# Optimization experiments

Hardware: AMD Instinct MI355X
Metric: run time of the kernel (lower is better)

## Reference

```python
import jax, jax.numpy as jnp
import numpy as np

B, S, D, H, KD, HID = 8, 1024, 512, 8, 64, 32


def setup_inputs() -> dict:
    key = jax.random.key(0)
    ks = jax.random.split(key, 13)
    s = 0.05
    return {
        "src": jax.random.normal(ks[0], (B, S, D), jnp.float32),
        "Wq": jax.random.normal(ks[1], (H, KD, D), jnp.float32) * s,
        "Wk": jax.random.normal(ks[2], (H, KD, D), jnp.float32) * s,
        "Wv": jax.random.normal(ks[3], (H, KD, D), jnp.float32) * s,
        "c_raw": jnp.ones((H,), jnp.float32),              # nn.Parameter(1.0) per head
        "L": jnp.full((H,), 2.0, jnp.float32),             # nn.Parameter(2.0) per head
        "w1": jax.random.normal(ks[4], (H, HID), jnp.float32) * s,   # Linear(1,HID) weight
        "b1": jax.random.normal(ks[5], (H, HID), jnp.float32) * s,
        "W2": jax.random.normal(ks[6], (H, HID, HID), jnp.float32) * s,  # [out,in]
        "b2": jax.random.normal(ks[7], (H, HID), jnp.float32) * s,
        "w3": jax.random.normal(ks[8], (H, HID), jnp.float32) * s,   # Linear(HID,1) weight
        "b3": jax.random.normal(ks[9], (H,), jnp.float32) * s,
        "Wo": jax.random.normal(ks[10], (D, D), jnp.float32) * s,
    }


def _gelu(x):
    return jax.nn.gelu(x, approximate=False)  # torch nn.GELU default (erf)


def reference(src, Wq, Wk, Wv, c_raw, L, w1, b1, W2, b2, w3, b3, Wo):
    Bc, Sc, Dc = src.shape
    Hh, Kd = Wq.shape[0], Wq.shape[1]
    # ---- FIRE bias: raw[i,j] = log1p(c*(i-j)) / log1p(c*max(L, i+1)) for j<i else 0
    ii = jnp.arange(Sc, dtype=jnp.float32)[:, None]   # [S,1]
    jj = jnp.arange(Sc, dtype=jnp.float32)[None, :]   # [1,S]
    d = ii - jj                                       # [S,S]
    c = jax.nn.softplus(c_raw)[:, None, None]         # [H,1,1]
    num = jnp.log1p(c * jnp.where(d > 0, d, 1.0)[None])          # safe for d<=0
    den = jnp.log1p(c * jnp.maximum(L[:, None, None], ii[None] + 1.0))
    raw = jnp.where(d[None] > 0, num / den, 0.0)      # [H,S,S]
    # ---- f_theta MLP applied elementwise (Linear(1,h)->GELU->Linear(h,h)->GELU->Linear(h,1))
    h1 = _gelu(raw[..., None] * w1[:, None, None, :] + b1[:, None, None, :])   # [H,S,S,HID]
    h2 = _gelu(jnp.einsum('hijk,hlk->hijl', h1, W2) + b2[:, None, None, :])    # [H,S,S,HID]
    bias = jnp.einsum('hijk,hk->hij', h2, w3) + b3[:, None, None]              # [H,S,S]
    # ---- causal mask (strict upper triangle -> -inf)
    causal = jnp.arange(Sc)[None, :] > jnp.arange(Sc)[:, None]
    bias = jnp.where(causal[None], -jnp.inf, bias)
    # ---- attention per head
    q = jnp.einsum('bsd,hkd->bhsk', src, Wq)
    k = jnp.einsum('bsd,hkd->bhsk', src, Wk)
    v = jnp.einsum('bsd,hkd->bhsk', src, Wv)
    logits = jnp.einsum('bhik,bhjk->bhij', q, k) / jnp.sqrt(jnp.float32(Kd)) + bias[None]
    attn = jax.nn.softmax(logits, axis=-1)
    o = jnp.einsum('bhij,bhjk->bhik', attn, v)        # [B,H,S,KD]
    o = jnp.transpose(o, (0, 2, 1, 3)).reshape(Bc, Sc, Hh * Kd)  # concat heads
    return o @ Wo.T
```

## Files before the change

kernel.cpp:

```cpp
#include <hip/hip_runtime.h>
#include <math.h>

#define S_LEN 1024
#define NHEAD 8
#define BATCH 8
#define KDIM  64
#define HID   32
#define NT    2048
#define LOG2E 1.4426950408889634f
#define TRI(q) ((q) * ((q) + 1) / 2)
#define PERM(m) (((m) & 0x20) | (((m) & 0x0C) << 1) | (((m) & 0x10) >> 2) | ((m) & 3))
#define SWZ(row) (((((row) >> 3) & 1) << 2) | ((row) & 3))

typedef __attribute__((ext_vector_type(8))) short bf16x8;
typedef __attribute__((ext_vector_type(4))) float f32x4;
typedef unsigned short ushort_t;

__device__ inline ushort_t f2bf(float f) {
  union { float f; unsigned u; } v; v.f = f;
  unsigned u = v.u;
  return (ushort_t)((u + 0x7FFFu + ((u >> 16) & 1u)) >> 16);
}
__device__ inline float bf2f(ushort_t u) {
  union { unsigned x; float f; } v; v.x = ((unsigned)u) << 16; return v.f;
}

__device__ inline void gl_lds16(const ushort_t* g, ushort_t* l) {
  __builtin_amdgcn_global_load_lds(
      (const __attribute__((address_space(1))) unsigned int*)g,
      (__attribute__((address_space(3))) unsigned int*)l, 16, 0, 0);
}

__global__ __launch_bounds__(256) void prep(
    const float* __restrict__ s, const float* __restrict__ wq,
    const float* __restrict__ wk, const float* __restrict__ wv,
    const float* __restrict__ wo,
    ushort_t* __restrict__ sb, ushort_t* __restrict__ wqb,
    ushort_t* __restrict__ wkb, ushort_t* __restrict__ wvb,
    ushort_t* __restrict__ wob,
    const float* __restrict__ c_raw, const float* __restrict__ Lp,
    const float* __restrict__ w1, const float* __restrict__ b1,
    const float* __restrict__ W2, const float* __restrict__ b2,
    const float* __restrict__ w3, const float* __restrict__ b3,
    float* __restrict__ num_g, float* __restrict__ rden_g,
    float* __restrict__ gtab_g) {
  __shared__ float h1s[8][33];
  const int bx = blockIdx.x;
  const int tid = threadIdx.x;
  if (bx < 5120) {
    const float* src; ushort_t* dst; int base; float scale = 1.0f;
    if (bx < 4096)      { src = s;  dst = sb;  base = bx; }
    else if (bx < 4352) { src = wq; dst = wqb; base = bx - 4096; scale = 0.125f * LOG2E; }
    else if (bx < 4608) { src = wk; dst = wkb; base = bx - 4352; }
    else if (bx < 4864) { src = wv; dst = wvb; base = bx - 4608; }
    else                { src = wo; dst = wob; base = bx - 4864; }
    const int i = (base * 256 + tid) * 4;
    float4 v = *(const float4*)&src[i];
    ushort4 o;
    o.x = f2bf(v.x * scale); o.y = f2bf(v.y * scale);
    o.z = f2bf(v.z * scale); o.w = f2bf(v.w * scale);
    *(ushort4*)&dst[i] = o;
  } else {
    const int idx = bx - 5120;
    const int h = idx / 257;
    const int xb = idx % 257;
    const float cr = c_raw[h];
    const float c = (cr > 20.f) ? cr : log1pf(expf(cr));
    const int gid = xb * 256 + tid;
    if (gid < S_LEN) {
      num_g[h * S_LEN + gid] = log1pf(c * (float)gid);
      rden_g[h * S_LEN + gid] = 1.0f / log1pf(c * fmaxf(Lp[h], (float)(gid + 1)));
    }
    const int pl = tid >> 5;
    const int j = tid & 31;
    const int pt = xb * 8 + pl;
    const float x = (float)pt * (1.0f / NT);
    float v = x * w1[h * HID + j] + b1[h * HID + j];
    h1s[pl][j] = 0.5f * v * (1.0f + erff(v * 0.70710678118f));
    __syncthreads();
    float sm = b2[h * HID + j];
    const float* w2r = W2 + ((size_t)(h * HID + j)) * HID;
    #pragma unroll
    for (int k = 0; k < HID; ++k) sm += w2r[k] * h1s[pl][k];
    float g = 0.5f * sm * (1.0f + erff(sm * 0.70710678118f));
    float y = w3[h * HID + j] * g;
    #pragma unroll
    for (int off = 1; off < 32; off <<= 1) y += __shfl_xor(y, off);
    if (j == 0 && pt <= NT) gtab_g[h * (NT + 1) + pt] = (y + b3[h]) * LOG2E;
  }
}

__device__ __forceinline__ void gemm_tile(
    ushort_t* sAB, const ushort_t* __restrict__ A, const ushort_t* __restrict__ Wp,
    void* __restrict__ outp, int mode, int m0, int n0, int tid) {
  ushort_t* sA = sAB;
  ushort_t* sB = sAB + 4096;
  const int lane = tid & 63, w = tid >> 6, quad = lane >> 4, l16 = lane & 15;
  f32x4 acc[4];
  #pragma unroll
  for (int nb = 0; nb < 4; ++nb) acc[nb] = (f32x4)0.0f;

  const int r8 = lane >> 3;
  const int gc = (lane & 7) ^ r8;
  const int sw = l16 & 7;

  for (int kt = 0; kt < 512; kt += 64) {
    __syncthreads();
    #pragma unroll
    for (int j = 0; j < 2; ++j) {
      const int row = w * 16 + j * 8 + r8;
      gl_lds16(&A[(size_t)(m0 + row) * 512 + kt + gc * 8], &sA[(w * 16 + j * 8) * 64]);
      gl_lds16(&Wp[(size_t)(n0 + row) * 512 + kt + gc * 8], &sB[(w * 16 + j * 8) * 64]);
    }
    __syncthreads();
    #pragma unroll
    for (int ks = 0; ks < 2; ++ks) {
      const int off = ((ks * 4 + quad) ^ sw) * 8;
      bf16x8 af = *(bf16x8*)&sA[(w * 16 + l16) * 64 + off];
      #pragma unroll
      for (int nb = 0; nb < 4; ++nb) {
        bf16x8 bfr = *(bf16x8*)&sB[(nb * 16 + l16) * 64 + off];
        acc[nb] = __builtin_amdgcn_mfma_f32_16x16x32_bf16(af, bfr, acc[nb], 0, 0, 0);
      }
    }
  }

  if (mode == 2) {
    __syncthreads();
    #pragma unroll
    for (int nb = 0; nb < 4; ++nb)
      #pragma unroll
      for (int r = 0; r < 4; ++r) {
        int nl = nb * 16 + l16;
        int ml = w * 16 + quad * 4 + r;
        sAB[nl * 64 + (((ml >> 3) ^ (nl & 7)) * 8) + (ml & 7)] = f2bf(acc[nb][r]);
      }
    __syncthreads();
    const int nl = tid >> 2, seg = tid & 3;
    const int ng = n0 + nl, hh = ng >> 6, kd = ng & 63;
    const int bb = m0 >> 10, sbase = m0 & 1023;
    ushort_t* vout = (ushort_t*)outp + (((size_t)(bb * NHEAD + hh)) * KDIM + kd) * S_LEN;
    #pragma unroll
    for (int c2 = 0; c2 < 2; ++c2) {
      int mc = seg * 2 + c2;
      bf16x8 vr = *(bf16x8*)&sAB[nl * 64 + ((mc ^ (nl & 7)) * 8)];
      *(bf16x8*)&vout[sbase + mc * 8] = vr;
    }
    return;
  }
  #pragma unroll
  for (int nb = 0; nb < 4; ++nb) {
    #pragma unroll
    for (int r = 0; r < 4; ++r) {
      int m = m0 + w * 16 + quad * 4 + r;
      int n = n0 + nb * 16 + l16;
      float v = acc[nb][r];
      if (mode == 1) {
        int bb = m >> 10, ss = m & 1023, hh = n >> 6, kd = n & 63;
        ((ushort_t*)outp)[(((size_t)(bb * NHEAD + hh)) * S_LEN + ss) * KDIM + kd] = f2bf(v);
      } else {
        ((float*)outp)[(size_t)m * 512 + n] = v;
      }
    }
  }
}

__global__ __launch_bounds__(256) void gemm_bias(
    const ushort_t* __restrict__ A,
    const ushort_t* __restrict__ W0, const ushort_t* __restrict__ W1,
    const ushort_t* __restrict__ W2w,
    void* __restrict__ out0, void* __restrict__ out1, void* __restrict__ out2,
    int scatter, int nGemm,
    const float* __restrict__ num_g, const float* __restrict__ rden_g,
    const float* __restrict__ gtab_g, ushort_t* __restrict__ biaspre) {
  __shared__ __align__(16) ushort_t sAB[8192];
  const int tid = threadIdx.x;
  if ((int)blockIdx.x < nGemm) {
    int z, tile;
    if (scatter) { z = blockIdx.x % 3; tile = blockIdx.x / 3; }
    else         { z = 0;              tile = blockIdx.x; }
    const int m0 = (tile & 127) * 64;
    const int n0 = (tile >> 7) * 64;
    const ushort_t* Wp = (z == 0) ? W0 : (z == 1) ? W1 : W2w;
    void* outp = (z == 0) ? out0 : (z == 1) ? out1 : out2;
    const int mode = scatter ? ((z == 2) ? 2 : 1) : 0;
    gemm_tile(sAB, A, Wp, outp, mode, m0, n0, tid);
  } else {
    const int idx = blockIdx.x - nGemm;
    const int h = idx / 68;
    const int pair = idx % 68;
    float* gtab_s = (float*)sAB;
    float* num_s = gtab_s + 2052;
    float* rden_s = num_s + 1024;
    for (int i = tid; i <= NT; i += 256) gtab_s[i] = gtab_g[h * (NT + 1) + i];
    for (int i = tid; i < S_LEN; i += 256) num_s[i] = num_g[h * S_LEN + i];
    const int sub = tid >> 7, tid2 = tid & 127;
    const int tileIdx = pair * 2 + sub;
    int qt = 0;
    while (TRI(qt + 1) <= tileIdx) ++qt;
    const int t = tileIdx - TRI(qt);
    if (tid2 < 64) rden_s[sub * 64 + tid2] = rden_g[h * S_LEN + qt * 64 + tid2];
    __syncthreads();
    const int w = tid2 >> 6, lane = tid2 & 63, quad = lane >> 4, l16 = lane & 15;
    ushort_t vals[32];
    #pragma unroll
    for (int qg = 0; qg < 2; ++qg) {
      const int iloc = w * 32 + qg * 16 + l16;
      const int i = qt * 64 + iloc;
      const float rden = rden_s[sub * 64 + iloc];
      #pragma unroll
      for (int nb = 0; nb < 4; ++nb)
        #pragma unroll
        for (int r = 0; r < 4; ++r) {
          const int m = nb * 16 + quad * 4 + r;
          const int j = t * 64 + PERM(m);
          ushort_t out;
          if (j > i) {
            out = 0xFF80;
          } else {
            const int d = i - j;
            float x = num_s[d] * rden;
            float tf = x * (float)NT;
            int it = (int)tf; it = it < (NT - 1) ? it : (NT - 1);
            float fr = tf - (float)it;
            float ga = gtab_s[it];
            out = f2bf(ga + (gtab_s[it + 1] - ga) * fr);
          }
          vals[qg * 16 + nb * 4 + r] = out;
        }
    }
    ushort_t* dst = &biaspre[((size_t)(h * 136 + tileIdx) * 128 + tid2) * 32];
    uint4 u[2];
    #pragma unroll
    for (int half = 0; half < 2; ++half) {
      #pragma unroll
      for (int v = 0; v < 8; ++v) ((ushort_t*)&u[0])[v] = vals[half * 16 + v];
      #pragma unroll
      for (int v = 0; v < 8; ++v) ((ushort_t*)&u[1])[v] = vals[half * 16 + 8 + v];
      *(uint4*)(dst + half * 16) = u[0];
      *(uint4*)(dst + half * 16 + 8) = u[1];
    }
  }
}

__global__ __launch_bounds__(128) void fire_attn_mfma(
    const ushort_t* __restrict__ Qg, const ushort_t* __restrict__ Kg,
    const ushort_t* __restrict__ Vtg, const ushort_t* __restrict__ biaspre,
    ushort_t* __restrict__ Ob) {
  __shared__ __align__(16) ushort_t Ks[64 * 64];
  __shared__ __align__(16) ushort_t Vt[64 * 64];
  const int tid = threadIdx.x;
  const int lane = tid & 63, w = tid >> 6, quad = lane >> 4, l16 = lane & 15;
  const int g = blockIdx.x >> 6;
  const int qt = (g < 8) ? (15 - g) : (g - 8);
  const int bh = blockIdx.x & 63, h = bh & 7, b = bh >> 3;

  bf16x8 q[2][2];
  {
    const size_t qb = (size_t)bh * S_LEN + qt * 64 + w * 32;
    #pragma unroll
    for (int qg = 0; qg < 2; ++qg)
      #pragma unroll
      for (int ks = 0; ks < 2; ++ks)
        q[qg][ks] = *(const bf16x8*)&Qg[(qb + qg * 16 + l16) * KDIM + ks * 32 + quad * 8];
  }

  const size_t kb = (size_t)bh * S_LEN * KDIM;
  const ushort_t* bptr = &biaspre[((size_t)(h * 136 + TRI(qt)) * 128 + tid) * 32];
  const int srow8 = lane >> 3;
  const int sc = lane & 7;

  f32x4 o[2][4];
  float ll[2] = {0.f, 0.f};
  #pragma unroll
  for (int qg = 0; qg < 2; ++qg)
    #pragma unroll
    for (int nb = 0; nb < 4; ++nb) o[qg][nb] = (f32x4)0.0f;

  for (int t = 0; t <= qt; ++t) {
    __syncthreads();
    #pragma unroll
    for (int j = 0; j < 4; ++j) {
      const int row = (w * 4 + j) * 8 + srow8;
      const int cc = sc ^ SWZ(row);
      gl_lds16(&Kg[kb + (size_t)(t * 64 + row) * 64 + cc * 8], &Ks[(w * 4 + j) * 512]);
      gl_lds16(&Vtg[kb + (size_t)row * 1024 + t * 64 + cc * 8], &Vt[(w * 4 + j) * 512]);
    }
    __syncthreads();

    uint4 bb0 = ((const uint4*)(bptr + (size_t)t * 4096))[0];
    uint4 bb1 = ((const uint4*)(bptr + (size_t)t * 4096))[1];
    uint4 bb2 = ((const uint4*)(bptr + (size_t)t * 4096))[2];
    uint4 bb3 = ((const uint4*)(bptr + (size_t)t * 4096))[3];

    f32x4 s[2][4];
    #pragma unroll
    for (int qg = 0; qg < 2; ++qg)
      #pragma unroll
      for (int nb = 0; nb < 4; ++nb) s[qg][nb] = (f32x4)0.0f;
    #pragma unroll
    for (int ks = 0; ks < 2; ++ks) {
      #pragma unroll
      for (int nb = 0; nb < 4; ++nb) {
        const int rk = PERM(nb * 16 + l16);
        bf16x8 ak = *(bf16x8*)&Ks[rk * 64 + (((ks * 4 + quad) ^ SWZ(rk)) * 8)];
        #pragma unroll
        for (int qg = 0; qg < 2; ++qg)
          s[qg][nb] = __builtin_amdgcn_mfma_f32_16x16x32_bf16(ak, q[qg][ks], s[qg][nb], 0, 0, 0);
      }
    }

    unsigned pk[2][4][2];
    #pragma unroll
    for (int qg = 0; qg < 2; ++qg) {
      #pragma unroll
      for (int nb = 0; nb < 4; ++nb) {
        const int v = qg * 16 + nb * 4;
        const uint4& bq = (v < 8) ? bb0 : (v < 16) ? bb1 : (v < 24) ? bb2 : bb3;
        const ushort_t* bu = (const ushort_t*)&bq;
        float p0 = __builtin_amdgcn_exp2f(s[qg][nb][0] + bf2f(bu[(v + 0) & 7]));
        float p1 = __builtin_amdgcn_exp2f(s[qg][nb][1] + bf2f(bu[(v + 1) & 7]));
        float p2 = __builtin_amdgcn_exp2f(s[qg][nb][2] + bf2f(bu[(v + 2) & 7]));
        float p3 = __builtin_amdgcn_exp2f(s[qg][nb][3] + bf2f(bu[(v + 3) & 7]));
        ll[qg] += (p0 + p1) + (p2 + p3);
        asm("v_cvt_pk_bf16_f32 %0, %1, %2" : "=v"(pk[qg][nb][0]) : "v"(p0), "v"(p1));
        asm("v_cvt_pk_bf16_f32 %0, %1, %2" : "=v"(pk[qg][nb][1]) : "v"(p2), "v"(p3));
      }
    }

    #pragma unroll
    for (int ks = 0; ks < 2; ++ks) {
      bf16x8 pf[2];
      #pragma unroll
      for (int qg = 0; qg < 2; ++qg) {
        union { bf16x8 v; unsigned u[4]; } pkx;
        pkx.u[0] = pk[qg][2 * ks][0];
        pkx.u[1] = pk[qg][2 * ks][1];
        pkx.u[2] = pk[qg][2 * ks + 1][0];
        pkx.u[3] = pk[qg][2 * ks + 1][1];
        pf[qg] = pkx.v;
      }
      #pragma unroll
      for (int nb = 0; nb < 4; ++nb) {
        const int rv = nb * 16 + l16;
        bf16x8 av = *(bf16x8*)&Vt[rv * 64 + (((ks * 4 + quad) ^ SWZ(rv)) * 8)];
        #pragma unroll
        for (int qg = 0; qg < 2; ++qg)
          o[qg][nb] = __builtin_amdgcn_mfma_f32_16x16x32_bf16(av, pf[qg], o[qg][nb], 0, 0, 0);
      }
    }
  }

  #pragma unroll
  for (int qg = 0; qg < 2; ++qg) {
    float rs = ll[qg];
    rs += __shfl_xor(rs, 16);
    rs += __shfl_xor(rs, 32);
    const float rl = 1.0f / rs;
    const size_t ob = ((size_t)(b * S_LEN + qt * 64 + w * 32 + qg * 16 + l16)) * 512 + h * KDIM;
    #pragma unroll
    for (int nb = 0; nb < 4; ++nb) {
      ushort4 ov;
      ov.x = f2bf(o[qg][nb][0] * rl);
      ov.y = f2bf(o[qg][nb][1] * rl);
      ov.z = f2bf(o[qg][nb][2] * rl);
      ov.w = f2bf(o[qg][nb][3] * rl);
      *(ushort4*)&Ob[ob + nb * 16 + quad * 4] = ov;
    }
  }
}

extern "C" void kernel_launch(void* const* d_in, const int* in_sizes, int n_in,
                              void* d_out, int out_size, void* d_ws, size_t ws_size,
                              hipStream_t stream) {
  const float* src   = (const float*)d_in[0];
  const float* Wq    = (const float*)d_in[1];
  const float* Wk    = (const float*)d_in[2];
  const float* Wv    = (const float*)d_in[3];
  const float* c_raw = (const float*)d_in[4];
  const float* Lp    = (const float*)d_in[5];
  const float* w1    = (const float*)d_in[6];
  const float* b1    = (const float*)d_in[7];
  const float* W2    = (const float*)d_in[8];
  const float* b2    = (const float*)d_in[9];
  const float* w3    = (const float*)d_in[10];
  const float* b3    = (const float*)d_in[11];
  const float* Wo    = (const float*)d_in[12];
  float* outp = (float*)d_out;

  const size_t SRC_E = 4194304;
  const size_t W_E   = 262144;
  const size_t QKV_E = 4194304;
  ushort_t* srcb = (ushort_t*)d_ws;
  ushort_t* Wqb  = srcb + SRC_E;
  ushort_t* Wkb  = Wqb + W_E;
  ushort_t* Wvb  = Wkb + W_E;
  ushort_t* Wob  = Wvb + W_E;
  ushort_t* Qb   = Wob + W_E;
  ushort_t* Kb   = Qb + QKV_E;
  ushort_t* Vtb  = Kb + QKV_E;
  ushort_t* Obb  = Vtb + QKV_E;
  ushort_t* biaspre = Obb + QKV_E;
  float* numb  = (float*)(biaspre + (size_t)NHEAD * 136 * 128 * 32);
  float* rdenb = numb + NHEAD * S_LEN;
  float* gtabb = rdenb + NHEAD * S_LEN;

  hipLaunchKernelGGL(prep, dim3(7176), dim3(256), 0, stream,
                     src, Wq, Wk, Wv, Wo, srcb, Wqb, Wkb, Wvb, Wob,
                     c_raw, Lp, w1, b1, W2, b2, w3, b3, numb, rdenb, gtabb);
  hipLaunchKernelGGL(gemm_bias, dim3(3616), dim3(256), 0, stream,
                     srcb, Wqb, Wkb, Wvb, (void*)Qb, (void*)Kb, (void*)Vtb,
                     1, 3072, numb, rdenb, gtabb, biaspre);
  hipLaunchKernelGGL(fire_attn_mfma, dim3(1024), dim3(128), 0, stream,
                     Qb, Kb, Vtb, biaspre, Obb);
  hipLaunchKernelGGL(gemm_bias, dim3(1024), dim3(256), 0, stream,
                     Obb, Wob, Wob, Wob, (void*)outp, (void*)outp, (void*)outp,
                     0, 1024, numb, rdenb, gtabb, biaspre);
}
```

Baseline: 167.0 us.

## Double-buffer LDS tiles in the projection GEMM and the attention K/V loop

Both the QKV/output GEMM tile loop and the attention K/V loop now use two LDS buffers. The next tile is issued with global-to-LDS loads while MFMA runs on the current tile, and each iteration needs one barrier instead of two. The aim is to hide global load latency behind compute. The cost is double the shared memory per block (32 KB in each kernel), which may lower the number of resident blocks per CU.

```diff
diff --git a/kernel.cpp b/kernel.cpp
--- a/kernel.cpp
+++ b/kernel.cpp
@@ -93,8 +93,6 @@
 __device__ __forceinline__ void gemm_tile(
     ushort_t* sAB, const ushort_t* __restrict__ A, const ushort_t* __restrict__ Wp,
     void* __restrict__ outp, int mode, int m0, int n0, int tid) {
-  ushort_t* sA = sAB;
-  ushort_t* sB = sAB + 4096;
   const int lane = tid & 63, w = tid >> 6, quad = lane >> 4, l16 = lane & 15;
   f32x4 acc[4];
   #pragma unroll
@@ -104,29 +102,38 @@
   const int gc = (lane & 7) ^ r8;
   const int sw = l16 & 7;
 
-  for (int kt = 0; kt < 512; kt += 64) {
-    __syncthreads();
+  auto stage = [&](int kt, int buf) {
+    ushort_t* sA = sAB + buf * 8192;
+    ushort_t* sB = sA + 4096;
     #pragma unroll
     for (int j = 0; j < 2; ++j) {
       const int row = w * 16 + j * 8 + r8;
       gl_lds16(&A[(size_t)(m0 + row) * 512 + kt + gc * 8], &sA[(w * 16 + j * 8) * 64]);
       gl_lds16(&Wp[(size_t)(n0 + row) * 512 + kt + gc * 8], &sB[(w * 16 + j * 8) * 64]);
     }
-    __syncthreads();
+  };
+
+  stage(0, 0);
+  __syncthreads();
+  for (int kt8 = 0; kt8 < 8; ++kt8) {
+    const int cur = kt8 & 1;
+    if (kt8 < 7) stage((kt8 + 1) * 64, cur ^ 1);
+    const ushort_t* sA = sAB + cur * 8192;
+    const ushort_t* sB = sA + 4096;
     #pragma unroll
     for (int ks = 0; ks < 2; ++ks) {
       const int off = ((ks * 4 + quad) ^ sw) * 8;
-      bf16x8 af = *(bf16x8*)&sA[(w * 16 + l16) * 64 + off];
+      bf16x8 af = *(const bf16x8*)&sA[(w * 16 + l16) * 64 + off];
       #pragma unroll
       for (int nb = 0; nb < 4; ++nb) {
-        bf16x8 bfr = *(bf16x8*)&sB[(nb * 16 + l16) * 64 + off];
+        bf16x8 bfr = *(const bf16x8*)&sB[(nb * 16 + l16) * 64 + off];
         acc[nb] = __builtin_amdgcn_mfma_f32_16x16x32_bf16(af, bfr, acc[nb], 0, 0, 0);
       }
     }
+    __syncthreads();
   }
 
   if (mode == 2) {
-    __syncthreads();
     #pragma unroll
     for (int nb = 0; nb < 4; ++nb)
       #pragma unroll
@@ -173,7 +180,7 @@
     int scatter, int nGemm,
     const float* __restrict__ num_g, const float* __restrict__ rden_g,
     const float* __restrict__ gtab_g, ushort_t* __restrict__ biaspre) {
-  __shared__ __align__(16) ushort_t sAB[8192];
+  __shared__ __align__(16) ushort_t sAB[16384];
   const int tid = threadIdx.x;
   if ((int)blockIdx.x < nGemm) {
     int z, tile;
@@ -247,8 +254,8 @@
     const ushort_t* __restrict__ Qg, const ushort_t* __restrict__ Kg,
     const ushort_t* __restrict__ Vtg, const ushort_t* __restrict__ biaspre,
     ushort_t* __restrict__ Ob) {
-  __shared__ __align__(16) ushort_t Ks[64 * 64];
-  __shared__ __align__(16) ushort_t Vt[64 * 64];
+  __shared__ __align__(16) ushort_t Ks[2 * 64 * 64];
+  __shared__ __align__(16) ushort_t Vt[2 * 64 * 64];
   const int tid = threadIdx.x;
   const int lane = tid & 63, w = tid >> 6, quad = lane >> 4, l16 = lane & 15;
   const int g = blockIdx.x >> 6;
@@ -270,6 +277,18 @@
   const int srow8 = lane >> 3;
   const int sc = lane & 7;
 
+  auto stageKV = [&](int t, int buf) {
+    #pragma unroll
+    for (int j = 0; j < 4; ++j) {
+      const int row = (w * 4 + j) * 8 + srow8;
+      const int cc = sc ^ SWZ(row);
+      gl_lds16(&Kg[kb + (size_t)(t * 64 + row) * 64 + cc * 8],
+               &Ks[buf * 4096 + (w * 4 + j) * 512]);
+      gl_lds16(&Vtg[kb + (size_t)row * 1024 + t * 64 + cc * 8],
+               &Vt[buf * 4096 + (w * 4 + j) * 512]);
+    }
+  };
+
   f32x4 o[2][4];
   float ll[2] = {0.f, 0.f};
   #pragma unroll
@@ -277,16 +296,13 @@
     #pragma unroll
     for (int nb = 0; nb < 4; ++nb) o[qg][nb] = (f32x4)0.0f;
 
+  stageKV(0, 0);
+  __syncthreads();
   for (int t = 0; t <= qt; ++t) {
-    __syncthreads();
-    #pragma unroll
-    for (int j = 0; j < 4; ++j) {
-      const int row = (w * 4 + j) * 8 + srow8;
-      const int cc = sc ^ SWZ(row);
-      gl_lds16(&Kg[kb + (size_t)(t * 64 + row) * 64 + cc * 8], &Ks[(w * 4 + j) * 512]);
-      gl_lds16(&Vtg[kb + (size_t)row * 1024 + t * 64 + cc * 8], &Vt[(w * 4 + j) * 512]);
-    }
-    __syncthreads();
+    const int cur = t & 1;
+    if (t < qt) stageKV(t + 1, cur ^ 1);
+    const ushort_t* Kc = Ks + cur * 4096;
+    const ushort_t* Vc = Vt + cur * 4096;
 
     uint4 bb0 = ((const uint4*)(bptr + (size_t)t * 4096))[0];
     uint4 bb1 = ((const uint4*)(bptr + (size_t)t * 4096))[1];
@@ -303,7 +319,7 @@
       #pragma unroll
       for (int nb = 0; nb < 4; ++nb) {
         const int rk = PERM(nb * 16 + l16);
-        bf16x8 ak = *(bf16x8*)&Ks[rk * 64 + (((ks * 4 + quad) ^ SWZ(rk)) * 8)];
+        bf16x8 ak = *(const bf16x8*)&Kc[rk * 64 + (((ks * 4 + quad) ^ SWZ(rk)) * 8)];
         #pragma unroll
         for (int qg = 0; qg < 2; ++qg)
           s[qg][nb] = __builtin_amdgcn_mfma_f32_16x16x32_bf16(ak, q[qg][ks], s[qg][nb], 0, 0, 0);
@@ -343,12 +359,13 @@
       #pragma unroll
       for (int nb = 0; nb < 4; ++nb) {
         const int rv = nb * 16 + l16;
-        bf16x8 av = *(bf16x8*)&Vt[rv * 64 + (((ks * 4 + quad) ^ SWZ(rv)) * 8)];
+        bf16x8 av = *(const bf16x8*)&Vc[rv * 64 + (((ks * 4 + quad) ^ SWZ(rv)) * 8)];
         #pragma unroll
         for (int qg = 0; qg < 2; ++qg)
           o[qg][nb] = __builtin_amdgcn_mfma_f32_16x16x32_bf16(av, pf[qg], o[qg][nb], 0, 0, 0);
       }
     }
+    __syncthreads();
   }
 
   #pragma unroll
```

Result: no change. 167.3 us (+0.2%).

## Split attention KV tiles across two wave pairs and merge partial sums in LDS

Applied to the files above, without the earlier changes.

The attention kernel now runs 256 threads per block. Two pairs of waves each handle half of the causal KV tiles for the same 64-row query tile, and the second pair's partial outputs and row sums are combined through shared memory at the end. The goal is to halve the serial KV loop length per block, which helps the long-tail query tiles and raises the number of waves available to hide latency. In exchange the block uses twice the LDS, adds a final reduction step, and leaves pair 1 idle on odd tile counts. This works without a running max because softmax here uses no max subtraction, so the partial sums add linearly.

```diff
diff --git a/kernel.cpp b/kernel.cpp
--- a/kernel.cpp
+++ b/kernel.cpp
@@ -23,6 +23,11 @@
 }
 __device__ inline float bf2f(ushort_t u) {
   union { unsigned x; float f; } v; v.x = ((unsigned)u) << 16; return v.f;
+}
+__device__ inline unsigned cvtpk_bf16(float lo, float hi) {
+  unsigned r;
+  asm("v_cvt_pk_bf16_f32 %0, %1, %2" : "=v"(r) : "v"(lo), "v"(hi));
+  return r;
 }
 
 __device__ inline void gl_lds16(const ushort_t* g, ushort_t* l) {
@@ -243,21 +248,23 @@
   }
 }
 
-__global__ __launch_bounds__(128) void fire_attn_mfma(
+__global__ __launch_bounds__(256) void fire_attn_mfma(
     const ushort_t* __restrict__ Qg, const ushort_t* __restrict__ Kg,
     const ushort_t* __restrict__ Vtg, const ushort_t* __restrict__ biaspre,
     ushort_t* __restrict__ Ob) {
-  __shared__ __align__(16) ushort_t Ks[64 * 64];
-  __shared__ __align__(16) ushort_t Vt[64 * 64];
+  __shared__ __align__(16) ushort_t sKV[16384];
   const int tid = threadIdx.x;
-  const int lane = tid & 63, w = tid >> 6, quad = lane >> 4, l16 = lane & 15;
+  const int lane = tid & 63, w = tid >> 6;
+  const int pair = w >> 1, wq = w & 1;
+  const int quad = lane >> 4, l16 = lane & 15;
   const int g = blockIdx.x >> 6;
   const int qt = (g < 8) ? (15 - g) : (g - 8);
   const int bh = blockIdx.x & 63, h = bh & 7, b = bh >> 3;
+  const int tid2 = wq * 64 + lane;
 
   bf16x8 q[2][2];
   {
-    const size_t qb = (size_t)bh * S_LEN + qt * 64 + w * 32;
+    const size_t qb = (size_t)bh * S_LEN + qt * 64 + wq * 32;
     #pragma unroll
     for (int qg = 0; qg < 2; ++qg)
       #pragma unroll
@@ -266,9 +273,22 @@
   }
 
   const size_t kb = (size_t)bh * S_LEN * KDIM;
-  const ushort_t* bptr = &biaspre[((size_t)(h * 136 + TRI(qt)) * 128 + tid) * 32];
+  const ushort_t* bptr = &biaspre[((size_t)(h * 136 + TRI(qt)) * 128 + tid2) * 32];
   const int srow8 = lane >> 3;
   const int sc = lane & 7;
+
+  ushort_t* Kp = sKV + pair * 4096;
+  ushort_t* Vp = sKV + 8192 + pair * 4096;
+
+  auto stageKV = [&](int t) {
+    #pragma unroll
+    for (int j = 0; j < 4; ++j) {
+      const int row = (wq * 4 + j) * 8 + srow8;
+      const int cc = sc ^ SWZ(row);
+      gl_lds16(&Kg[kb + (size_t)(t * 64 + row) * 64 + cc * 8], &Kp[(wq * 4 + j) * 512]);
+      gl_lds16(&Vtg[kb + (size_t)row * 1024 + t * 64 + cc * 8], &Vp[(wq * 4 + j) * 512]);
+    }
+  };
 
   f32x4 o[2][4];
   float ll[2] = {0.f, 0.f};
@@ -277,95 +297,116 @@
     #pragma unroll
     for (int nb = 0; nb < 4; ++nb) o[qg][nb] = (f32x4)0.0f;
 
-  for (int t = 0; t <= qt; ++t) {
-    __syncthreads();
-    #pragma unroll
-    for (int j = 0; j < 4; ++j) {
-      const int row = (w * 4 + j) * 8 + srow8;
-      const int cc = sc ^ SWZ(row);
-      gl_lds16(&Kg[kb + (size_t)(t * 64 + row) * 64 + cc * 8], &Ks[(w * 4 + j) * 512]);
-      gl_lds16(&Vtg[kb + (size_t)row * 1024 + t * 64 + cc * 8], &Vt[(w * 4 + j) * 512]);
-    }
-    __syncthreads();
-
-    uint4 bb0 = ((const uint4*)(bptr + (size_t)t * 4096))[0];
-    uint4 bb1 = ((const uint4*)(bptr + (size_t)t * 4096))[1];
-    uint4 bb2 = ((const uint4*)(bptr + (size_t)t * 4096))[2];
-    uint4 bb3 = ((const uint4*)(bptr + (size_t)t * 4096))[3];
-
-    f32x4 s[2][4];
+  const int hA = (qt + 2) >> 1;
+  for (int it = 0; it < hA; ++it) {
+    const int t = pair ? (hA + it) : it;
+    const bool act = (!pair) || (t <= qt);
+    if (act) stageKV(t);
+    __syncthreads();
+    if (act) {
+      uint4 bb0 = ((const uint4*)(bptr + (size_t)t * 4096))[0];
+      uint4 bb1 = ((const uint4*)(bptr + (size_t)t * 4096))[1];
+      uint4 bb2 = ((const uint4*)(bptr + (size_t)t * 4096))[2];
+      uint4 bb3 = ((const uint4*)(bptr + (size_t)t * 4096))[3];
+
+      f32x4 s[2][4];
+      #pragma unroll
+      for (int qg = 0; qg < 2; ++qg)
+        #pragma unroll
+        for (int nb = 0; nb < 4; ++nb) s[qg][nb] = (f32x4)0.0f;
+      #pragma unroll
+      for (int ks = 0; ks < 2; ++ks) {
+        #pragma unroll
+        for (int nb = 0; nb < 4; ++nb) {
+          const int rk = PERM(nb * 16 + l16);
+          bf16x8 ak = *(const bf16x8*)&Kp[rk * 64 + (((ks * 4 + quad) ^ SWZ(rk)) * 8)];
+          #pragma unroll
+          for (int qg = 0; qg < 2; ++qg)
+            s[qg][nb] = __builtin_amdgcn_mfma_f32_16x16x32_bf16(ak, q[qg][ks], s[qg][nb], 0, 0, 0);
+        }
+      }
+
+      unsigned pk[2][4][2];
+      #pragma unroll
+      for (int qg = 0; qg < 2; ++qg) {
+        #pragma unroll
+        for (int nb = 0; nb < 4; ++nb) {
+          const int v = qg * 16 + nb * 4;
+          const uint4& bq = (v < 8) ? bb0 : (v < 16) ? bb1 : (v < 24) ? bb2 : bb3;
+          const ushort_t* bu = (const ushort_t*)&bq;
+          float p0 = __builtin_amdgcn_exp2f(s[qg][nb][0] + bf2f(bu[(v + 0) & 7]));
+          float p1 = __builtin_amdgcn_exp2f(s[qg][nb][1] + bf2f(bu[(v + 1) & 7]));
+          float p2 = __builtin_amdgcn_exp2f(s[qg][nb][2] + bf2f(bu[(v + 2) & 7]));
+          float p3 = __builtin_amdgcn_exp2f(s[qg][nb][3] + bf2f(bu[(v + 3) & 7]));
+          ll[qg] += (p0 + p1) + (p2 + p3);
+          pk[qg][nb][0] = cvtpk_bf16(p0, p1);
+          pk[qg][nb][1] = cvtpk_bf16(p2, p3);
+        }
+      }
+
+      #pragma unroll
+      for (int ks = 0; ks < 2; ++ks) {
+        bf16x8 pf[2];
+        #pragma unroll
+        for (int qg = 0; qg < 2; ++qg) {
+          union { bf16x8 v; unsigned u[4]; } pkx;
+          pkx.u[0] = pk[qg][2 * ks][0];
+          pkx.u[1] = pk[qg][2 * ks][1];
+          pkx.u[2] = pk[qg][2 * ks + 1][0];
+          pkx.u[3] = pk[qg][2 * ks + 1][1];
+          pf[qg] = pkx.v;
+        }
+        #pragma unroll
+        for (int nb = 0; nb < 4; ++nb) {
+          const int rv = nb * 16 + l16;
+          bf16x8 av = *(const bf16x8*)&Vp[rv * 64 + (((ks * 4 + quad) ^ SWZ(rv)) * 8)];
+          #pragma unroll
+          for (int qg = 0; qg < 2; ++qg)
+            o[qg][nb] = __builtin_amdgcn_mfma_f32_16x16x32_bf16(av, pf[qg], o[qg][nb], 0, 0, 0);
+        }
+      }
+    }
+    __syncthreads();
+  }
+
+  float* cb = (float*)sKV;
+  if (pair == 1) {
+    float* my = cb + tid2 * 34;
     #pragma unroll
     for (int qg = 0; qg < 2; ++qg)
       #pragma unroll
-      for (int nb = 0; nb < 4; ++nb) s[qg][nb] = (f32x4)0.0f;
-    #pragma unroll
-    for (int ks = 0; ks < 2; ++ks) {
+      for (int nb = 0; nb < 4; ++nb)
+        #pragma unroll
+        for (int r = 0; r < 4; ++r) my[qg * 16 + nb * 4 + r] = o[qg][nb][r];
+    my[32] = ll[0]; my[33] = ll[1];
+  }
+  __syncthreads();
+  if (pair == 0) {
+    const float* pb = cb + tid2 * 34;
+    #pragma unroll
+    for (int qg = 0; qg < 2; ++qg)
+      #pragma unroll
+      for (int nb = 0; nb < 4; ++nb)
+        #pragma unroll
+        for (int r = 0; r < 4; ++r) o[qg][nb][r] += pb[qg * 16 + nb * 4 + r];
+    ll[0] += pb[32]; ll[1] += pb[33];
+
+    #pragma unroll
+    for (int qg = 0; qg < 2; ++qg) {
+      float rs = ll[qg];
+      rs += __shfl_xor(rs, 16);
+      rs += __shfl_xor(rs, 32);
+      const float rl = 1.0f / rs;
+      const size_t ob = ((size_t)(b * S_LEN + qt * 64 + wq * 32 + qg * 16 + l16)) * 512 + h * KDIM;
       #pragma unroll
       for (int nb = 0; nb < 4; ++nb) {
-        const int rk = PERM(nb * 16 + l16);
-        bf16x8 ak = *(bf16x8*)&Ks[rk * 64 + (((ks * 4 + quad) ^ SWZ(rk)) * 8)];
-        #pragma unroll
-        for (int qg = 0; qg < 2; ++qg)
-          s[qg][nb] = __builtin_amdgcn_mfma_f32_16x16x32_bf16(ak, q[qg][ks], s[qg][nb], 0, 0, 0);
-      }
-    }
-
-    unsigned pk[2][4][2];
-    #pragma unroll
-    for (int qg = 0; qg < 2; ++qg) {
-      #pragma unroll
-      for (int nb = 0; nb < 4; ++nb) {
-        const int v = qg * 16 + nb * 4;
-        const uint4& bq = (v < 8) ? bb0 : (v < 16) ? bb1 : (v < 24) ? bb2 : bb3;
-        const ushort_t* bu = (const ushort_t*)&bq;
-        float p0 = __builtin_amdgcn_exp2f(s[qg][nb][0] + bf2f(bu[(v + 0) & 7]));
-        float p1 = __builtin_amdgcn_exp2f(s[qg][nb][1] + bf2f(bu[(v + 1) & 7]));
-        float p2 = __builtin_amdgcn_exp2f(s[qg][nb][2] + bf2f(bu[(v + 2) & 7]));
-        float p3 = __builtin_amdgcn_exp2f(s[qg][nb][3] + bf2f(bu[(v + 3) & 7]));
-        ll[qg] += (p0 + p1) + (p2 + p3);
-        asm("v_cvt_pk_bf16_f32 %0, %1, %2" : "=v"(pk[qg][nb][0]) : "v"(p0), "v"(p1));
-        asm("v_cvt_pk_bf16_f32 %0, %1, %2" : "=v"(pk[qg][nb][1]) : "v"(p2), "v"(p3));
-      }
-    }
-
-    #pragma unroll
-    for (int ks = 0; ks < 2; ++ks) {
-      bf16x8 pf[2];
-      #pragma unroll
-      for (int qg = 0; qg < 2; ++qg) {
-        union { bf16x8 v; unsigned u[4]; } pkx;
-        pkx.u[0] = pk[qg][2 * ks][0];
-        pkx.u[1] = pk[qg][2 * ks][1];
-        pkx.u[2] = pk[qg][2 * ks + 1][0];
-        pkx.u[3] = pk[qg][2 * ks + 1][1];
-        pf[qg] = pkx.v;
-      }
-      #pragma unroll
-      for (int nb = 0; nb < 4; ++nb) {
-        const int rv = nb * 16 + l16;
-        bf16x8 av = *(bf16x8*)&Vt[rv * 64 + (((ks * 4 + quad) ^ SWZ(rv)) * 8)];
-        #pragma unroll
-        for (int qg = 0; qg < 2; ++qg)
-          o[qg][nb] = __builtin_amdgcn_mfma_f32_16x16x32_bf16(av, pf[qg], o[qg][nb], 0, 0, 0);
-      }
-    }
-  }
-
-  #pragma unroll
-  for (int qg = 0; qg < 2; ++qg) {
-    float rs = ll[qg];
-    rs += __shfl_xor(rs, 16);
-    rs += __shfl_xor(rs, 32);
-    const float rl = 1.0f / rs;
-    const size_t ob = ((size_t)(b * S_LEN + qt * 64 + w * 32 + qg * 16 + l16)) * 512 + h * KDIM;
-    #pragma unroll
-    for (int nb = 0; nb < 4; ++nb) {
-      ushort4 ov;
-      ov.x = f2bf(o[qg][nb][0] * rl);
-      ov.y = f2bf(o[qg][nb][1] * rl);
-      ov.z = f2bf(o[qg][nb][2] * rl);
-      ov.w = f2bf(o[qg][nb][3] * rl);
-      *(ushort4*)&Ob[ob + nb * 16 + quad * 4] = ov;
+        ushort4 ov;
+        ov.x = f2bf(o[qg][nb][0] * rl);
+        ov.y = f2bf(o[qg][nb][1] * rl);
+        ov.z = f2bf(o[qg][nb][2] * rl);
+        ov.w = f2bf(o[qg][nb][3] * rl);
+        *(ushort4*)&Ob[ob + nb * 16 + quad * 4] = ov;
+      }
     }
   }
 }
@@ -411,7 +452,7 @@
   hipLaunchKernelGGL(gemm_bias, dim3(3616), dim3(256), 0, stream,
                      srcb, Wqb, Wkb, Wvb, (void*)Qb, (void*)Kb, (void*)Vtb,
                      1, 3072, numb, rdenb, gtabb, biaspre);
-  hipLaunchKernelGGL(fire_attn_mfma, dim3(1024), dim3(128), 0, stream,
+  hipLaunchKernelGGL(fire_attn_mfma, dim3(1024), dim3(256), 0, stream,
                      Qb, Kb, Vtb, biaspre, Obb);
   hipLaunchKernelGGL(gemm_bias, dim3(1024), dim3(256), 0, stream,
                      Obb, Wob, Wob, Wob, (void*)outp, (void*)outp, (void*)outp,
```

After: 160.5 us. 3.9% less time.
